# Optimization experiments

Measured on AMD Instinct MI355X. Metric: run time of the kernel, lower is better.

## Reference

```python
import jax, jax.numpy as jnp
import numpy as np

MS_TOKEN_SIZE = (1, 2, 4, 8, 16)  # divisor scales -> 'area' == exact average pooling


def _area_down(x, ph, pw):
    # F.interpolate(mode='area') with divisor target sizes == block average pool
    B, C, H, W = x.shape
    return x.reshape(B, C, ph, H // ph, pw, W // pw).mean(axis=(3, 5))


def _bicubic_up(x, H, W):
    # F.interpolate(mode='bicubic', align_corners=False) ~ jax.image.resize 'cubic'
    B, C, h, w = x.shape
    return jax.image.resize(x, (B, C, H, W), method='cubic')


def setup_inputs() -> dict:
    key = jax.random.key(0)
    k1, k2 = jax.random.split(key)
    z_enc = jax.random.normal(k1, (64, 32, 16, 16), dtype=jnp.float32)
    emb_weight = jax.random.normal(k2, (4096, 32), dtype=jnp.float32) * 0.01
    return {"z_enc": z_enc, "emb_weight": emb_weight}


def reference(z_enc, emb_weight):
    # obtain_multiscale_quantized_feature: multiscale residual VQ.
    # phi is identity (not defined in the provided source).
    B, C, H, W = z_enc.shape
    levels = len(MS_TOKEN_SIZE)
    z_rest = jax.lax.stop_gradient(z_enc)  # z_enc.detach()
    z_dec = jnp.zeros_like(z_rest)
    w_ng = jax.lax.stop_gradient(emb_weight)  # .data in distance computation
    w_sq = jnp.sum(w_ng * w_ng, axis=1)  # [K]
    ret = []
    for level, pn in enumerate(MS_TOKEN_SIZE):
        ph = pw = pn
        zd = _area_down(z_rest, ph, pw) if level != levels - 1 else z_rest
        zflat = zd.transpose(0, 2, 3, 1).reshape(-1, C)  # [B*ph*pw, C]
        # ||z||^2 + ||e||^2 - 2 z.e^T
        dist = (jnp.sum(zflat * zflat, axis=1, keepdims=True) + w_sq
                - 2.0 * (zflat @ w_ng.T))  # [B*ph*pw, K]
        token = jnp.argmin(dist, axis=1).reshape(B, ph, pw)
        z_up = jnp.take(emb_weight, token, axis=0).transpose(0, 3, 1, 2)  # [B,C,ph,pw]
        if level != levels - 1:
            z_up = _bicubic_up(z_up, H, W)
        z_dec = z_dec + z_up
        z_rest = z_rest - jax.lax.stop_gradient(z_up)
        ret.append(z_dec)
    return jnp.stack(ret)  # [levels, B, C, H, W]
```

## Files before the change

### kernel.cpp

```cpp
#include <hip/hip_runtime.h>

#define NB 64
#define NC 32
#define PLANE 256
#define NK 4096

__device__ __forceinline__ float cubic_w(float x) {
    x = fabsf(x);
    if (x >= 2.f) return 0.f;
    if (x >= 1.f) return ((-0.5f * x + 2.5f) * x - 4.f) * x + 2.f;
    return ((1.5f * x - 2.5f) * x) * x + 1.f;
}

template <int PN>
__device__ __forceinline__ void taps(int o, float* w, int& i0, int& n) {
    float sf = (o + 0.5f) * ((float)PN / 16.f) - 0.5f;
    int lo = (int)floorf(sf) - 1;
    int hi = lo + 3;
    if (lo < 0) lo = 0;
    if (hi > PN - 1) hi = PN - 1;
    n = hi - lo + 1;
    i0 = lo;
    float tot = 0.f;
    for (int i = 0; i < n; i++) {
        float ww = cubic_w(sf - (float)(lo + i));
        w[i] = ww;
        tot += ww;
    }
    float inv = 1.f / tot;
    for (int i = 0; i < n; i++) w[i] *= inv;
}

#define FMA4(D, A, B)                                                          \
    D = __builtin_fmaf((A).x, (B).x, D); D = __builtin_fmaf((A).y, (B).y, D);  \
    D = __builtin_fmaf((A).z, (B).z, D); D = __builtin_fmaf((A).w, (B).w, D)
#define DOT32(D)                                                               \
    FMA4(D, z0, w0); FMA4(D, z1, w1); FMA4(D, z2, w2); FMA4(D, z3, w3);        \
    FMA4(D, z4, w4); FMA4(D, z5, w5); FMA4(D, z6, w6); FMA4(D, z7, w7)
#define DOT32_2(DA, DB)                                                        \
    FMA4(DA, a0, w0); FMA4(DB, b0, w0); FMA4(DA, a1, w1); FMA4(DB, b1, w1);    \
    FMA4(DA, a2, w2); FMA4(DB, b2, w2); FMA4(DA, a3, w3); FMA4(DB, b3, w3);    \
    FMA4(DA, a4, w4); FMA4(DB, b4, w4); FMA4(DA, a5, w5); FMA4(DB, b5, w5);    \
    FMA4(DA, a6, w6); FMA4(DB, b6, w6); FMA4(DA, a7, w7); FMA4(DB, b7, w7)

__device__ __forceinline__ float pairwise_zsq(float4 z0, float4 z1, float4 z2,
                                              float4 z3, float4 z4, float4 z5,
                                              float4 z6, float4 z7) {
#define SQ_(a) __fmul_rn((a), (a))
#define R4_(a, b, c, d) \
    __fadd_rn(__fadd_rn(__fadd_rn(SQ_(a), SQ_(b)), SQ_(c)), SQ_(d))
    float r0 = R4_(z0.x, z2.x, z4.x, z6.x);
    float r1 = R4_(z0.y, z2.y, z4.y, z6.y);
    float r2 = R4_(z0.z, z2.z, z4.z, z6.z);
    float r3 = R4_(z0.w, z2.w, z4.w, z6.w);
    float r4 = R4_(z1.x, z3.x, z5.x, z7.x);
    float r5 = R4_(z1.y, z3.y, z5.y, z7.y);
    float r6 = R4_(z1.z, z3.z, z5.z, z7.z);
    float r7 = R4_(z1.w, z3.w, z5.w, z7.w);
    return __fadd_rn(__fadd_rn(__fadd_rn(r0, r1), __fadd_rn(r2, r3)),
                     __fadd_rn(__fadd_rn(r4, r5), __fadd_rn(r6, r7)));
#undef R4_
#undef SQ_
}

__global__ void __launch_bounds__(256) init_kernel(
    const float* __restrict__ z_enc, const float* __restrict__ emb,
    float* __restrict__ zflat0, float* __restrict__ wsq) {
    int t = threadIdx.x;
    __shared__ float p[4];
    for (int i = 0; i < 4; i++) {
        int bc = blockIdx.x * 4 + i;
        float v = z_enc[bc * PLANE + t];
        for (int o = 32; o > 0; o >>= 1) v += __shfl_down(v, o, 64);
        if ((t & 63) == 0) p[t >> 6] = v;
        __syncthreads();
        if (t == 0) zflat0[bc] = (p[0] + p[1] + p[2] + p[3]) * (1.f / 256.f);
        __syncthreads();
    }
    int k = blockIdx.x * 8 + (t >> 5);
    int c = t & 31;
    float e = emb[k * 32 + c];
    float s = __fmul_rn(e, e);
    for (int o = 16; o > 0; o >>= 1) s += __shfl_down(s, o, 32);
    if (c == 0) wsq[k] = s;
}

template <int CPK>
__global__ void __launch_bounds__(256, 4) part2_kernel(
    const float* __restrict__ zflat, const float* __restrict__ emb,
    const float* __restrict__ wsq, float* __restrict__ cand_d,
    int* __restrict__ cand_i, int T) {
    int wave = threadIdx.x >> 6, lane = threadIdx.x & 63;
    int tokA = (blockIdx.x * 4 + wave) * 128 + lane;
    int tokB = tokA + 64;
    int KS = gridDim.y;
    int k0 = blockIdx.y * CPK;
    const float4* za = (const float4*)(zflat + (size_t)tokA * 32);
    const float4* zb = (const float4*)(zflat + (size_t)tokB * 32);
    float4 a0 = za[0], a1 = za[1], a2 = za[2], a3 = za[3];
    float4 a4 = za[4], a5 = za[5], a6 = za[6], a7 = za[7];
    float4 b0 = zb[0], b1 = zb[1], b2 = zb[2], b3 = zb[3];
    float4 b4 = zb[4], b5 = zb[5], b6 = zb[6], b7 = zb[7];
    float zsqA = pairwise_zsq(a0, a1, a2, a3, a4, a5, a6, a7);
    float zsqB = pairwise_zsq(b0, b1, b2, b3, b4, b5, b6, b7);

    float bestA = 1e30f, bestB = 1e30f;
    int biA = 0, biB = 0;
#pragma unroll 2
    for (int k = k0; k < k0 + CPK; k++) {
        const float4* wr = (const float4*)emb + (size_t)k * 8;
        float4 w0 = wr[0], w1 = wr[1], w2 = wr[2], w3 = wr[3];
        float4 w4 = wr[4], w5 = wr[5], w6 = wr[6], w7 = wr[7];
        float wk = wsq[k];
        float dotA = 0.f, dotB = 0.f;
        DOT32_2(dotA, dotB);
        float dA = __fsub_rn(__fadd_rn(zsqA, wk), __fmul_rn(2.f, dotA));
        float dB = __fsub_rn(__fadd_rn(zsqB, wk), __fmul_rn(2.f, dotB));
        if (dA < bestA) { bestA = dA; biA = k; }
        if (dB < bestB) { bestB = dB; biB = k; }
    }
    cand_d[(size_t)tokA * KS + blockIdx.y] = bestA;
    cand_i[(size_t)tokA * KS + blockIdx.y] = biA;
    cand_d[(size_t)tokB * KS + blockIdx.y] = bestB;
    cand_i[(size_t)tokB * KS + blockIdx.y] = biB;
}

template <int KPL>
__global__ void __launch_bounds__(256, 4) partk_kernel(
    const float* __restrict__ zflat, const float* __restrict__ emb,
    const float* __restrict__ wsq, float* __restrict__ cand_d,
    int* __restrict__ cand_i, int T) {
    int wave = threadIdx.x >> 6, lane = threadIdx.x & 63;
    int tok = blockIdx.x * 4 + wave;
    int KS = gridDim.y;
    int kbase = blockIdx.y * (KPL * 64);
    const float4* zr = (const float4*)(zflat + (size_t)tok * 32);
    float4 z0 = zr[0], z1 = zr[1], z2 = zr[2], z3 = zr[3];
    float4 z4 = zr[4], z5 = zr[5], z6 = zr[6], z7 = zr[7];
    float zsq = pairwise_zsq(z0, z1, z2, z3, z4, z5, z6, z7);

    float best = 1e30f;
    int bi = 0;
#pragma unroll
    for (int j = 0; j < KPL; j++) {
        int k = kbase + j * 64 + lane;
        const float4* wr = (const float4*)emb + (size_t)k * 8;
        float4 w0 = wr[0], w1 = wr[1], w2 = wr[2], w3 = wr[3];
        float4 w4 = wr[4], w5 = wr[5], w6 = wr[6], w7 = wr[7];
        float dot = 0.f;
        DOT32(dot);
        float d = __fsub_rn(__fadd_rn(zsq, wsq[k]), __fmul_rn(2.f, dot));
        if (d < best) { best = d; bi = k; }
    }
    for (int off = 32; off > 0; off >>= 1) {
        float od = __shfl_down(best, off, 64);
        int oi = __shfl_down(bi, off, 64);
        if (od < best || (od == best && oi < bi)) { best = od; bi = oi; }
    }
    if (lane == 0) {
        cand_d[(size_t)tok * KS + blockIdx.y] = best;
        cand_i[(size_t)tok * KS + blockIdx.y] = bi;
    }
}

__global__ void __launch_bounds__(256) combine_wave(
    const float* __restrict__ cand_d, const int* __restrict__ cand_i,
    const float* __restrict__ emb, float* __restrict__ zq, int T, int KS) {
    int wgl = blockIdx.x * 4 + (threadIdx.x >> 6);
    int lane = threadIdx.x & 63;
    int nw = gridDim.x * 4;
    for (int tok = wgl; tok < T; tok += nw) {
        float best = 1e30f;
        int bi = 0x7fffffff;
        for (int s = lane; s < KS; s += 64) {
            float d = cand_d[(size_t)tok * KS + s];
            int i = cand_i[(size_t)tok * KS + s];
            if (d < best || (d == best && i < bi)) { best = d; bi = i; }
        }
        for (int off = 32; off > 0; off >>= 1) {
            float od = __shfl_down(best, off, 64);
            int oi = __shfl_down(bi, off, 64);
            if (od < best || (od == best && oi < bi)) { best = od; bi = oi; }
        }
        bi = __shfl(bi, 0, 64);
        if (lane < 8) {
            ((float4*)zq)[(size_t)tok * 8 + lane] =
                ((const float4*)emb)[(size_t)bi * 8 + lane];
        }
    }
}

template <int PN, int PN_NEXT>
__global__ void __launch_bounds__(256) apply_kernel(
    const float* __restrict__ zrest_in, const float* __restrict__ zq,
    float* __restrict__ out_lvl, const float* __restrict__ out_prev,
    float* __restrict__ zrest_out, float* __restrict__ zflat_next) {
    __shared__ float rest[PLANE];
    int t = threadIdx.x;
    int h = t >> 4, w = t & 15;

    float wy[4], wx[4];
    int iy0 = 0, ny = 0, jx0 = 0, nx = 0;
    if constexpr (PN != 16) {
        taps<PN>(h, wy, iy0, ny);
        taps<PN>(w, wx, jx0, nx);
    }

    for (int it = 0; it < 4; it++) {
        int bc = blockIdx.x * 4 + it;
        int b = bc >> 5, c = bc & 31;

        float zup;
        if constexpr (PN == 16) {
            zup = zq[(size_t)(((b * 16 + h) * 16 + w)) * 32 + c];
        } else {
            zup = 0.f;
            for (int e = 0; e < nx; e++) {
                float colacc = 0.f;
                for (int a = 0; a < ny; a++)
                    colacc += wy[a] * zq[(size_t)((b * PN + iy0 + a) * PN + (jx0 + e)) * 32 + c];
                zup += wx[e] * colacc;
            }
        }
        int idx = bc * PLANE + t;
        float prev = out_prev ? out_prev[idx] : 0.f;
        out_lvl[idx] = __fadd_rn(prev, zup);

        if (zflat_next) {
            float rv = __fsub_rn(zrest_in[idx], zup);
            rest[t] = rv;
            if (zrest_out) zrest_out[idx] = rv;
            __syncthreads();
            constexpr int S = 16 / PN_NEXT;
            if (t < PN_NEXT * PN_NEXT) {
                int i = t / PN_NEXT, j = t % PN_NEXT;
                float s = 0.f;
                for (int di = 0; di < S; di++)
                    for (int dj = 0; dj < S; dj++)
                        s = __fadd_rn(s, rest[(i * S + di) * 16 + (j * S + dj)]);
                zflat_next[(size_t)((b * PN_NEXT + i) * PN_NEXT + j) * 32 + c] =
                    s * (1.f / (float)(S * S));
            }
            __syncthreads();
        }
    }
}

extern "C" void kernel_launch(void* const* d_in, const int* in_sizes, int n_in,
                              void* d_out, int out_size, void* d_ws, size_t ws_size,
                              hipStream_t stream) {
    const float* z_enc = (const float*)d_in[0];
    const float* emb   = (const float*)d_in[1];
    float* out = (float*)d_out;
    float* ws = (float*)d_ws;

    float* wsq    = ws;
    float* zflat  = wsq + NK;
    float* zq     = zflat + 524288;
    float* zrest  = zq + 524288;
    float* cand_d = zrest + 524288;
    int*   cand_i = (int*)(cand_d + 524288);

    const int LVL = NB * NC * PLANE;

    init_kernel<<<512, 256, 0, stream>>>(z_enc, emb, zflat, wsq);

    partk_kernel<4><<<dim3(16, 16), 256, 0, stream>>>(zflat, emb, wsq, cand_d, cand_i, 64);
    combine_wave<<<16, 256, 0, stream>>>(cand_d, cand_i, emb, zq, 64, 16);
    apply_kernel<1, 2><<<512, 256, 0, stream>>>(z_enc, zq, out, nullptr, zrest, zflat);

    partk_kernel<4><<<dim3(64, 16), 256, 0, stream>>>(zflat, emb, wsq, cand_d, cand_i, 256);
    combine_wave<<<64, 256, 0, stream>>>(cand_d, cand_i, emb, zq, 256, 16);
    apply_kernel<2, 4><<<512, 256, 0, stream>>>(zrest, zq, out + LVL, out, zrest, zflat);

    part2_kernel<8><<<dim3(2, 512), 256, 0, stream>>>(zflat, emb, wsq, cand_d, cand_i, 1024);
    combine_wave<<<256, 256, 0, stream>>>(cand_d, cand_i, emb, zq, 1024, 512);
    apply_kernel<4, 8><<<512, 256, 0, stream>>>(zrest, zq, out + 2 * LVL, out + LVL, zrest, zflat);

    part2_kernel<32><<<dim3(8, 128), 256, 0, stream>>>(zflat, emb, wsq, cand_d, cand_i, 4096);
    combine_wave<<<256, 256, 0, stream>>>(cand_d, cand_i, emb, zq, 4096, 128);
    apply_kernel<8, 16><<<512, 256, 0, stream>>>(zrest, zq, out + 3 * LVL, out + 2 * LVL, zrest, zflat);

    part2_kernel<128><<<dim3(32, 32), 256, 0, stream>>>(zflat, emb, wsq, cand_d, cand_i, 16384);
    combine_wave<<<256, 256, 0, stream>>>(cand_d, cand_i, emb, zq, 16384, 32);
    apply_kernel<16, 16><<<512, 256, 0, stream>>>(zrest, zq, out + 4 * LVL, out + 3 * LVL, nullptr, nullptr);
}
```

Measured before the change: 276.0 us.

## Fuse argmin, combine and apply stages per batch to cut kernel launches

Levels 0 and 1 now run search, selection and upsample/residual update in one kernel per level, one block per batch, with no candidate split. Levels 2-4 merge the candidate combine with the apply step into a per-batch kernel. The init kernel is remapped to one plane per block. This removes about eight launches and their global round trips. In exchange, apply work runs on only 64 blocks that each loop over 32 channels with block barriers, which cuts parallelism for the memory-bound apply phase.

```diff
diff --git a/kernel.cpp b/kernel.cpp
--- a/kernel.cpp
+++ b/kernel.cpp
@@ -66,23 +66,171 @@
 __global__ void __launch_bounds__(256) init_kernel(
     const float* __restrict__ z_enc, const float* __restrict__ emb,
     float* __restrict__ zflat0, float* __restrict__ wsq) {
+    int bc = blockIdx.x;
     int t = threadIdx.x;
+    float v = z_enc[bc * PLANE + t];
+    for (int o = 32; o > 0; o >>= 1) v += __shfl_down(v, o, 64);
     __shared__ float p[4];
-    for (int i = 0; i < 4; i++) {
-        int bc = blockIdx.x * 4 + i;
-        float v = z_enc[bc * PLANE + t];
-        for (int o = 32; o > 0; o >>= 1) v += __shfl_down(v, o, 64);
-        if ((t & 63) == 0) p[t >> 6] = v;
-        __syncthreads();
-        if (t == 0) zflat0[bc] = (p[0] + p[1] + p[2] + p[3]) * (1.f / 256.f);
-        __syncthreads();
-    }
-    int k = blockIdx.x * 8 + (t >> 5);
-    int c = t & 31;
-    float e = emb[k * 32 + c];
-    float s = __fmul_rn(e, e);
-    for (int o = 16; o > 0; o >>= 1) s += __shfl_down(s, o, 32);
-    if (c == 0) wsq[k] = s;
+    if ((t & 63) == 0) p[t >> 6] = v;
+    __syncthreads();
+    if (t == 0) zflat0[bc] = (p[0] + p[1] + p[2] + p[3]) * (1.f / 256.f);
+    if (t < 64) {
+        int k = 2 * bc + (t >> 5);
+        int c = t & 31;
+        float e = emb[k * 32 + c];
+        float s = __fmul_rn(e, e);
+        for (int o = 16; o > 0; o >>= 1) s += __shfl_down(s, o, 32);
+        if (c == 0) wsq[k] = s;
+    }
+}
+
+template <int PN, int PN_NEXT>
+__device__ __forceinline__ void dev_apply_batch(int b, int t,
+    const float* __restrict__ zrest_in, const float* __restrict__ zq,
+    float* __restrict__ out_lvl, const float* __restrict__ out_prev,
+    float* __restrict__ zrest_out, float* __restrict__ zflat_next,
+    float* rest) {
+    int h = t >> 4, w = t & 15;
+    float wy[4], wx[4];
+    int iy0 = 0, ny = 0, jx0 = 0, nx = 0;
+    if constexpr (PN != 16) {
+        taps<PN>(h, wy, iy0, ny);
+        taps<PN>(w, wx, jx0, nx);
+    }
+    for (int c = 0; c < 32; c++) {
+        int bc = b * 32 + c;
+        float zup;
+        if constexpr (PN == 16) {
+            zup = zq[(size_t)(((b * 16 + h) * 16 + w)) * 32 + c];
+        } else {
+            zup = 0.f;
+            for (int e = 0; e < nx; e++) {
+                float colacc = 0.f;
+                for (int a = 0; a < ny; a++)
+                    colacc += wy[a] * zq[(size_t)((b * PN + iy0 + a) * PN + (jx0 + e)) * 32 + c];
+                zup += wx[e] * colacc;
+            }
+        }
+        int idx = bc * PLANE + t;
+        float prev = out_prev ? out_prev[idx] : 0.f;
+        out_lvl[idx] = __fadd_rn(prev, zup);
+
+        if (zflat_next) {
+            float rv = __fsub_rn(zrest_in[idx], zup);
+            rest[t] = rv;
+            if (zrest_out) zrest_out[idx] = rv;
+            __syncthreads();
+            constexpr int S = 16 / PN_NEXT;
+            if (t < PN_NEXT * PN_NEXT) {
+                int i = t / PN_NEXT, j = t % PN_NEXT;
+                float s = 0.f;
+                for (int di = 0; di < S; di++)
+                    for (int dj = 0; dj < S; dj++)
+                        s = __fadd_rn(s, rest[(i * S + di) * 16 + (j * S + dj)]);
+                zflat_next[(size_t)((b * PN_NEXT + i) * PN_NEXT + j) * 32 + c] =
+                    s * (1.f / (float)(S * S));
+            }
+            __syncthreads();
+        }
+    }
+}
+
+__global__ void __launch_bounds__(256) fused_l0(
+    const float* __restrict__ z_enc, const float* __restrict__ emb,
+    const float* __restrict__ wsq, const float* __restrict__ zflat,
+    float* __restrict__ zq, float* __restrict__ out,
+    float* __restrict__ zrest, float* __restrict__ zflat_sc) {
+    int b = blockIdx.x, t = threadIdx.x;
+    int wave = t >> 6, lane = t & 63;
+    __shared__ float sd[4];
+    __shared__ int si[4];
+    __shared__ int sbi;
+    __shared__ float rest[PLANE];
+
+    const float4* zr = (const float4*)(zflat + (size_t)b * 32);
+    float4 z0 = zr[0], z1 = zr[1], z2 = zr[2], z3 = zr[3];
+    float4 z4 = zr[4], z5 = zr[5], z6 = zr[6], z7 = zr[7];
+    float zsq = pairwise_zsq(z0, z1, z2, z3, z4, z5, z6, z7);
+
+    float best = 1e30f;
+    int bi = 0;
+    int kbase = wave * 1024;
+#pragma unroll
+    for (int j = 0; j < 16; j++) {
+        int k = kbase + j * 64 + lane;
+        const float4* wr = (const float4*)emb + (size_t)k * 8;
+        float4 w0 = wr[0], w1 = wr[1], w2 = wr[2], w3 = wr[3];
+        float4 w4 = wr[4], w5 = wr[5], w6 = wr[6], w7 = wr[7];
+        float dot = 0.f;
+        DOT32(dot);
+        float d = __fsub_rn(__fadd_rn(zsq, wsq[k]), __fmul_rn(2.f, dot));
+        if (d < best) { best = d; bi = k; }
+    }
+    for (int off = 32; off > 0; off >>= 1) {
+        float od = __shfl_down(best, off, 64);
+        int oi = __shfl_down(bi, off, 64);
+        if (od < best || (od == best && oi < bi)) { best = od; bi = oi; }
+    }
+    if (lane == 0) { sd[wave] = best; si[wave] = bi; }
+    __syncthreads();
+    if (t == 0) {
+        float bb = 1e30f;
+        int ii = 0x7fffffff;
+        for (int s = 0; s < 4; s++) {
+            float d = sd[s];
+            int i2 = si[s];
+            if (d < bb || (d == bb && i2 < ii)) { bb = d; ii = i2; }
+        }
+        sbi = ii;
+    }
+    __syncthreads();
+    if (t < 32) zq[(size_t)b * 32 + t] = emb[(size_t)sbi * 32 + t];
+    __syncthreads();
+
+    dev_apply_batch<1, 2>(b, t, z_enc, zq, out, nullptr, zrest, zflat_sc, rest);
+}
+
+__global__ void __launch_bounds__(256) fused_l1(
+    const float* __restrict__ emb, const float* __restrict__ wsq,
+    const float* __restrict__ zflat_sc, float* __restrict__ zq,
+    float* __restrict__ out_lvl, const float* __restrict__ out_prev,
+    float* __restrict__ zrest, float* __restrict__ zflat) {
+    int b = blockIdx.x, t = threadIdx.x;
+    int wave = t >> 6, lane = t & 63;
+    __shared__ float rest[PLANE];
+    int tok = b * 4 + wave;
+
+    const float4* zr = (const float4*)(zflat_sc + (size_t)tok * 32);
+    float4 z0 = zr[0], z1 = zr[1], z2 = zr[2], z3 = zr[3];
+    float4 z4 = zr[4], z5 = zr[5], z6 = zr[6], z7 = zr[7];
+    float zsq = pairwise_zsq(z0, z1, z2, z3, z4, z5, z6, z7);
+
+    float best = 1e30f;
+    int bi = 0;
+#pragma unroll 4
+    for (int j = 0; j < 64; j++) {
+        int k = j * 64 + lane;
+        const float4* wr = (const float4*)emb + (size_t)k * 8;
+        float4 w0 = wr[0], w1 = wr[1], w2 = wr[2], w3 = wr[3];
+        float4 w4 = wr[4], w5 = wr[5], w6 = wr[6], w7 = wr[7];
+        float dot = 0.f;
+        DOT32(dot);
+        float d = __fsub_rn(__fadd_rn(zsq, wsq[k]), __fmul_rn(2.f, dot));
+        if (d < best) { best = d; bi = k; }
+    }
+    for (int off = 32; off > 0; off >>= 1) {
+        float od = __shfl_down(best, off, 64);
+        int oi = __shfl_down(bi, off, 64);
+        if (od < best || (od == best && oi < bi)) { best = od; bi = oi; }
+    }
+    bi = __shfl(bi, 0, 64);
+    if (lane < 8) {
+        ((float4*)zq)[(size_t)tok * 8 + lane] =
+            ((const float4*)emb)[(size_t)bi * 8 + lane];
+    }
+    __syncthreads();
+
+    dev_apply_batch<2, 4>(b, t, zrest, zq, out_lvl, out_prev, zrest, zflat, rest);
 }
 
 template <int CPK>
@@ -125,51 +273,20 @@
     cand_i[(size_t)tokB * KS + blockIdx.y] = biB;
 }
 
-template <int KPL>
-__global__ void __launch_bounds__(256, 4) partk_kernel(
-    const float* __restrict__ zflat, const float* __restrict__ emb,
-    const float* __restrict__ wsq, float* __restrict__ cand_d,
-    int* __restrict__ cand_i, int T) {
-    int wave = threadIdx.x >> 6, lane = threadIdx.x & 63;
-    int tok = blockIdx.x * 4 + wave;
-    int KS = gridDim.y;
-    int kbase = blockIdx.y * (KPL * 64);
-    const float4* zr = (const float4*)(zflat + (size_t)tok * 32);
-    float4 z0 = zr[0], z1 = zr[1], z2 = zr[2], z3 = zr[3];
-    float4 z4 = zr[4], z5 = zr[5], z6 = zr[6], z7 = zr[7];
-    float zsq = pairwise_zsq(z0, z1, z2, z3, z4, z5, z6, z7);
-
-    float best = 1e30f;
-    int bi = 0;
-#pragma unroll
-    for (int j = 0; j < KPL; j++) {
-        int k = kbase + j * 64 + lane;
-        const float4* wr = (const float4*)emb + (size_t)k * 8;
-        float4 w0 = wr[0], w1 = wr[1], w2 = wr[2], w3 = wr[3];
-        float4 w4 = wr[4], w5 = wr[5], w6 = wr[6], w7 = wr[7];
-        float dot = 0.f;
-        DOT32(dot);
-        float d = __fsub_rn(__fadd_rn(zsq, wsq[k]), __fmul_rn(2.f, dot));
-        if (d < best) { best = d; bi = k; }
-    }
-    for (int off = 32; off > 0; off >>= 1) {
-        float od = __shfl_down(best, off, 64);
-        int oi = __shfl_down(bi, off, 64);
-        if (od < best || (od == best && oi < bi)) { best = od; bi = oi; }
-    }
-    if (lane == 0) {
-        cand_d[(size_t)tok * KS + blockIdx.y] = best;
-        cand_i[(size_t)tok * KS + blockIdx.y] = bi;
-    }
-}
-
-__global__ void __launch_bounds__(256) combine_wave(
+template <int PN, int PN_NEXT, int KS>
+__global__ void __launch_bounds__(256) ca_kernel(
     const float* __restrict__ cand_d, const int* __restrict__ cand_i,
-    const float* __restrict__ emb, float* __restrict__ zq, int T, int KS) {
-    int wgl = blockIdx.x * 4 + (threadIdx.x >> 6);
-    int lane = threadIdx.x & 63;
-    int nw = gridDim.x * 4;
-    for (int tok = wgl; tok < T; tok += nw) {
+    const float* __restrict__ emb, float* __restrict__ zq,
+    const float* __restrict__ zrest_in, float* __restrict__ out_lvl,
+    const float* __restrict__ out_prev, float* __restrict__ zrest_out,
+    float* __restrict__ zflat_next) {
+    int b = blockIdx.x, t = threadIdx.x;
+    int wave = t >> 6, lane = t & 63;
+    __shared__ float rest[PLANE];
+    constexpr int PT = PN * PN;
+
+    for (int tl = wave; tl < PT; tl += 4) {
+        int tok = b * PT + tl;
         float best = 1e30f;
         int bi = 0x7fffffff;
         for (int s = lane; s < KS; s += 64) {
@@ -188,62 +305,10 @@
                 ((const float4*)emb)[(size_t)bi * 8 + lane];
         }
     }
-}
-
-template <int PN, int PN_NEXT>
-__global__ void __launch_bounds__(256) apply_kernel(
-    const float* __restrict__ zrest_in, const float* __restrict__ zq,
-    float* __restrict__ out_lvl, const float* __restrict__ out_prev,
-    float* __restrict__ zrest_out, float* __restrict__ zflat_next) {
-    __shared__ float rest[PLANE];
-    int t = threadIdx.x;
-    int h = t >> 4, w = t & 15;
-
-    float wy[4], wx[4];
-    int iy0 = 0, ny = 0, jx0 = 0, nx = 0;
-    if constexpr (PN != 16) {
-        taps<PN>(h, wy, iy0, ny);
-        taps<PN>(w, wx, jx0, nx);
-    }
-
-    for (int it = 0; it < 4; it++) {
-        int bc = blockIdx.x * 4 + it;
-        int b = bc >> 5, c = bc & 31;
-
-        float zup;
-        if constexpr (PN == 16) {
-            zup = zq[(size_t)(((b * 16 + h) * 16 + w)) * 32 + c];
-        } else {
-            zup = 0.f;
-            for (int e = 0; e < nx; e++) {
-                float colacc = 0.f;
-                for (int a = 0; a < ny; a++)
-                    colacc += wy[a] * zq[(size_t)((b * PN + iy0 + a) * PN + (jx0 + e)) * 32 + c];
-                zup += wx[e] * colacc;
-            }
-        }
-        int idx = bc * PLANE + t;
-        float prev = out_prev ? out_prev[idx] : 0.f;
-        out_lvl[idx] = __fadd_rn(prev, zup);
-
-        if (zflat_next) {
-            float rv = __fsub_rn(zrest_in[idx], zup);
-            rest[t] = rv;
-            if (zrest_out) zrest_out[idx] = rv;
-            __syncthreads();
-            constexpr int S = 16 / PN_NEXT;
-            if (t < PN_NEXT * PN_NEXT) {
-                int i = t / PN_NEXT, j = t % PN_NEXT;
-                float s = 0.f;
-                for (int di = 0; di < S; di++)
-                    for (int dj = 0; dj < S; dj++)
-                        s = __fadd_rn(s, rest[(i * S + di) * 16 + (j * S + dj)]);
-                zflat_next[(size_t)((b * PN_NEXT + i) * PN_NEXT + j) * 32 + c] =
-                    s * (1.f / (float)(S * S));
-            }
-            __syncthreads();
-        }
-    }
+    __syncthreads();
+
+    dev_apply_batch<PN, PN_NEXT>(b, t, zrest_in, zq, out_lvl, out_prev,
+                                 zrest_out, zflat_next, rest);
 }
 
 extern "C" void kernel_launch(void* const* d_in, const int* in_sizes, int n_in,
@@ -263,25 +328,21 @@
 
     const int LVL = NB * NC * PLANE;
 
-    init_kernel<<<512, 256, 0, stream>>>(z_enc, emb, zflat, wsq);
-
-    partk_kernel<4><<<dim3(16, 16), 256, 0, stream>>>(zflat, emb, wsq, cand_d, cand_i, 64);
-    combine_wave<<<16, 256, 0, stream>>>(cand_d, cand_i, emb, zq, 64, 16);
-    apply_kernel<1, 2><<<512, 256, 0, stream>>>(z_enc, zq, out, nullptr, zrest, zflat);
-
-    partk_kernel<4><<<dim3(64, 16), 256, 0, stream>>>(zflat, emb, wsq, cand_d, cand_i, 256);
-    combine_wave<<<64, 256, 0, stream>>>(cand_d, cand_i, emb, zq, 256, 16);
-    apply_kernel<2, 4><<<512, 256, 0, stream>>>(zrest, zq, out + LVL, out, zrest, zflat);
+    init_kernel<<<2048, 256, 0, stream>>>(z_enc, emb, zflat, wsq);
+
+    fused_l0<<<64, 256, 0, stream>>>(z_enc, emb, wsq, zflat, zq, out, zrest, cand_d);
+
+    fused_l1<<<64, 256, 0, stream>>>(emb, wsq, cand_d, zq, out + LVL, out, zrest, zflat);
 
     part2_kernel<8><<<dim3(2, 512), 256, 0, stream>>>(zflat, emb, wsq, cand_d, cand_i, 1024);
-    combine_wave<<<256, 256, 0, stream>>>(cand_d, cand_i, emb, zq, 1024, 512);
-    apply_kernel<4, 8><<<512, 256, 0, stream>>>(zrest, zq, out + 2 * LVL, out + LVL, zrest, zflat);
+    ca_kernel<4, 8, 512><<<64, 256, 0, stream>>>(cand_d, cand_i, emb, zq,
+        zrest, out + 2 * LVL, out + LVL, zrest, zflat);
 
     part2_kernel<32><<<dim3(8, 128), 256, 0, stream>>>(zflat, emb, wsq, cand_d, cand_i, 4096);
-    combine_wave<<<256, 256, 0, stream>>>(cand_d, cand_i, emb, zq, 4096, 128);
-    apply_kernel<8, 16><<<512, 256, 0, stream>>>(zrest, zq, out + 3 * LVL, out + 2 * LVL, zrest, zflat);
+    ca_kernel<8, 16, 128><<<64, 256, 0, stream>>>(cand_d, cand_i, emb, zq,
+        zrest, out + 3 * LVL, out + 2 * LVL, zrest, zflat);
 
     part2_kernel<128><<<dim3(32, 32), 256, 0, stream>>>(zflat, emb, wsq, cand_d, cand_i, 16384);
-    combine_wave<<<256, 256, 0, stream>>>(cand_d, cand_i, emb, zq, 16384, 32);
-    apply_kernel<16, 16><<<512, 256, 0, stream>>>(zrest, zq, out + 4 * LVL, out + 3 * LVL, nullptr, nullptr);
-}
+    ca_kernel<16, 16, 32><<<64, 256, 0, stream>>>(cand_d, cand_i, emb, zq,
+        zrest, out + 4 * LVL, out + 3 * LVL, nullptr, nullptr);
+}
```

Measured after the change: 575.4 us. +108.5%, slower.
